# Optimization experiments

Measured on AMD Instinct MI355X. Metric: run time of the kernel, lower is better.

Reference implementation:

```python
import jax, jax.numpy as jnp
import numpy as np
from jax import lax

CUT = 20            # voxel grid per side, hard-coded in the torch module
N, P, OP = 32, 8192, 2048


def _w(key, shape, fan_in):
    return jax.random.normal(key, shape, dtype=jnp.float32) * np.float32(1.0 / np.sqrt(fan_in))


def setup_inputs() -> dict:
    key = jax.random.key(0)
    ks = jax.random.split(key, 20)
    inp = {}
    inp["sc"] = jax.random.uniform(ks[0], (N, P, 2), dtype=jnp.float32, minval=-0.5, maxval=0.5)
    inp["oc"] = jax.random.uniform(ks[1], (N, OP, 2), dtype=jnp.float32, minval=-0.5, maxval=0.5)
    inp["pos"] = jax.random.uniform(ks[2], (N, 2), dtype=jnp.float32, minval=-0.5, maxval=0.5)
    # voxel PointNet MLP (1x1 Conv1d == per-point linear)
    inp["mlp_w1"] = _w(ks[3], (128, 2), 2);        inp["mlp_b1"] = jnp.zeros((128,), jnp.float32)
    inp["mlp_w2"] = _w(ks[4], (256, 128), 128);    inp["mlp_b2"] = jnp.zeros((256,), jnp.float32)
    # dense conv pyramid
    inp["conv1_w"] = _w(ks[5], (512, 256, 3, 3), 256 * 9);   inp["conv1_b"] = jnp.zeros((512,), jnp.float32)
    inp["conv2_w"] = _w(ks[6], (1024, 512, 3, 3), 512 * 9);  inp["conv2_b"] = jnp.zeros((1024,), jnp.float32)
    inp["convt_w"] = _w(ks[7], (512, 1024, 2, 2), 1024 * 4); inp["convt_b"] = jnp.zeros((512,), jnp.float32)
    # object set-abstraction (stack of 1x1 Conv1d)
    inp["sa_w1"] = _w(ks[8], (64, 2), 2);          inp["sa_b1"] = jnp.zeros((64,), jnp.float32)
    inp["sa_w2"] = _w(ks[9], (128, 64), 64);       inp["sa_b2"] = jnp.zeros((128,), jnp.float32)
    inp["sa_w3"] = _w(ks[10], (256, 128), 128);    inp["sa_b3"] = jnp.zeros((256,), jnp.float32)
    inp["sa_w4"] = _w(ks[11], (512, 256), 256);    inp["sa_b4"] = jnp.zeros((512,), jnp.float32)
    # per-cell classifier
    inp["cls_w1"] = _w(ks[12], (1024, 1538), 1538); inp["cls_b1"] = jnp.zeros((1024,), jnp.float32)
    inp["cls_w2"] = _w(ks[13], (256, 1024), 1024);  inp["cls_b2"] = jnp.zeros((256,), jnp.float32)
    inp["cls_w3"] = _w(ks[14], (1, 256), 256);      inp["cls_b3"] = jnp.zeros((1,), jnp.float32)
    return inp


def _conv2d(x, w, b):
    y = lax.conv_general_dilated(x, w, (1, 1), ((1, 1), (1, 1)),
                                 dimension_numbers=("NCHW", "OIHW", "NCHW"))
    return y + b[None, :, None, None]


def _maxpool2(x):
    return lax.reduce_window(x, -jnp.inf, lax.max, (1, 1, 2, 2), (1, 1, 2, 2), "VALID")


def reference(sc, oc, pos,
              mlp_w1, mlp_b1, mlp_w2, mlp_b2,
              conv1_w, conv1_b, conv2_w, conv2_b, convt_w, convt_b,
              sa_w1, sa_b1, sa_w2, sa_b2, sa_w3, sa_b3, sa_w4, sa_b4,
              cls_w1, cls_b1, cls_w2, cls_b2, cls_w3, cls_b3):
    n = sc.shape[0]
    # ---- fused voxelization + PointNet + scatter-max (replaces triple loop) ----
    x, y = sc[..., 0], sc[..., 1]
    # torch condition: cut[i] < x <= cut[i+1] on linspace(-0.5, 0.5, 21)
    bi = jnp.clip(jnp.ceil((x + 0.5) * CUT) - 1, 0, CUT - 1).astype(jnp.int32)
    bj = jnp.clip(jnp.ceil((y + 0.5) * CUT) - 1, 0, CUT - 1).astype(jnp.int32)
    valid = (x > -0.5) & (x <= 0.5) & (y > -0.5) & (y <= 0.5)
    ci = -0.5 + (bi.astype(sc.dtype) + 0.5) / CUT   # voxel center x
    cj = -0.5 + (bj.astype(sc.dtype) + 0.5) / CUT   # voxel center y
    pc = jnp.stack([x - ci, y - cj], axis=-1).reshape(-1, 2)        # [n*P, 2]
    h = jax.nn.relu(pc @ mlp_w1.T + mlp_b1)
    feat = jax.nn.relu(h @ mlp_w2.T + mlp_b2)                       # [n*P, 256]
    seg = jnp.where(valid,
                    jnp.arange(n, dtype=jnp.int32)[:, None] * (CUT * CUT) + bi * CUT + bj,
                    n * CUT * CUT).reshape(-1)                      # invalid -> dummy bin
    nseg = n * CUT * CUT + 1
    mx = jax.ops.segment_max(feat, seg, num_segments=nseg)
    cnt = jax.ops.segment_sum(jnp.ones((n * P,), jnp.float32), seg, num_segments=nseg)
    vox = jnp.where(cnt[:, None] > 0, mx, 0.0)[: n * CUT * CUT]     # empty voxels stay 0
    vox = vox.reshape(n, CUT, CUT, 256).transpose(0, 3, 1, 2)       # [n,256,20,20]
    # ---- dense conv pyramid ----
    f1 = _maxpool2(jax.nn.relu(_conv2d(vox, conv1_w, conv1_b)))     # [n,512,10,10]
    f2 = _maxpool2(jax.nn.relu(_conv2d(f1, conv2_w, conv2_b)))      # [n,1024,5,5]
    f3 = lax.conv_transpose(f2, convt_w, (2, 2), "VALID",
                            dimension_numbers=("NCHW", "OIHW", "NCHW"))
    f3 = f3 + convt_b[None, :, None, None]                          # [n,512,10,10]
    scene = jnp.concatenate([f1, f3], axis=1)                       # [n,1024,10,10]
    S = scene.shape[2]
    scene_flat = scene.reshape(n, 1024, S * S)
    # ---- object PointNet (1x1 convs == per-point linears) + global max ----
    obj_c = oc - jnp.mean(oc, axis=1, keepdims=True)                # [n,OP,2]
    g = jax.nn.relu(obj_c @ sa_w1.T + sa_b1)
    g = jax.nn.relu(g @ sa_w2.T + sa_b2)
    g = jax.nn.relu(g @ sa_w3.T + sa_b3)
    g = jax.nn.relu(g @ sa_w4.T + sa_b4)                            # [n,OP,512]
    obj = jnp.max(g, axis=1)                                        # [n,512]
    obj_tiled = jnp.broadcast_to(obj[:, :, None], (n, 512, S * S))
    # ---- relative position grid ----
    c = -0.5 + (jnp.arange(S, dtype=sc.dtype) + 0.5) / S
    rel_x = jnp.broadcast_to(pos[:, 0][:, None, None] - c[None, :, None], (n, S, S))
    rel_y = jnp.broadcast_to(pos[:, 1][:, None, None] - c[None, None, :], (n, S, S))
    rel = jnp.stack([rel_x, rel_y], axis=1).reshape(n, 2, S * S)
    # ---- per-cell classifier ----
    cin = jnp.concatenate([scene_flat, obj_tiled, rel], axis=1).transpose(0, 2, 1)  # [n,100,1538]
    h = jax.nn.relu(cin @ cls_w1.T + cls_b1)
    h = jax.nn.relu(h @ cls_w2.T + cls_b2)
    return h @ cls_w3.T + cls_b3                                    # [n,100,1]
```

## Files before the change

kernel.cpp:

```cpp
#include <hip/hip_runtime.h>

#define NB 32
#define PP 8192
#define OPP 2048

typedef _Float16 f16;
typedef f16 half8 __attribute__((ext_vector_type(8)));
typedef f16 half4 __attribute__((ext_vector_type(4)));
typedef f16 half2v __attribute__((ext_vector_type(2)));
typedef float f32x4 __attribute__((ext_vector_type(4)));

#define MFMA16(a, b, c) __builtin_amdgcn_mfma_f32_16x16x32_f16(a, b, c, 0, 0, 0)

__global__ __launch_bounds__(256) void prepfuse_k(
    const float* __restrict__ mlp_w2, const float* __restrict__ sa_w2,
    const float* __restrict__ sa_w3, const float* __restrict__ sa_w4,
    const float* __restrict__ cls_w2, const float* __restrict__ cls_w1,
    const float* __restrict__ convt_w, const float* __restrict__ conv1_w,
    const float* __restrict__ conv2_w, const float* __restrict__ oc,
    f16* __restrict__ mw2h, f16* __restrict__ saw2h, f16* __restrict__ saw3h,
    f16* __restrict__ saw4h, f16* __restrict__ cw2h, f16* __restrict__ cw1h,
    f16* __restrict__ ctwh, f16* __restrict__ w1h, f16* __restrict__ w2h,
    float* __restrict__ ocm) {
  __shared__ float tile[512 * 9];
  int bb = blockIdx.x, t = threadIdx.x;
  if (bb < 2048) {
    constexpr int B0 = 8192, B1 = B0 + 2048, B2 = B1 + 8192, B3 = B2 + 32768, B4 = B3 + 65536;
    constexpr int C1e = B4 + 524288;
    constexpr int TOT = C1e + 2097152;
    for (int idx = bb * 256 + t; idx < TOT; idx += 2048 * 256) {
      if (idx < B4) {
        const float* in; f16* out; int off;
        if (idx < B0)      { in = mlp_w2; out = mw2h;  off = idx; }
        else if (idx < B1) { in = sa_w2;  out = saw2h; off = idx - B0; }
        else if (idx < B2) { in = sa_w3;  out = saw3h; off = idx - B1; }
        else if (idx < B3) { in = sa_w4;  out = saw4h; off = idx - B2; }
        else               { in = cls_w2; out = cw2h;  off = idx - B3; }
        float4 v = ((const float4*)in)[off];
        half4 h; h.x = (f16)v.x; h.y = (f16)v.y; h.z = (f16)v.z; h.w = (f16)v.w;
        ((half4*)out)[off] = h;
      } else if (idx < C1e) {
        int i = idx - B4;
        int co = i >> 9, k2 = i & 511;
        float2 v = *(const float2*)(cls_w1 + (size_t)co * 1538 + k2 * 2);
        half2v h = {(f16)v.x, (f16)v.y};
        *(half2v*)(cw1h + (size_t)co * 1024 + k2 * 2) = h;
      } else {
        int i = idx - C1e;
        int j = i & 7, l = (i >> 3) & 63, kb = (i >> 9) & 31, nb = i >> 14;
        int n16 = l & 15, quad = l >> 4;
        int np = nb * 16 + n16;
        int k = kb * 32 + quad * 8 + j;
        int p = np >> 9, o = np & 511;
        ctwh[i] = (f16)convt_w[((size_t)o * 1024 + k) * 4 + (3 - p)];
      }
    }
  } else if (bb < 2080) {
    float* sx = tile; float* sy = tile + 256;
    int n = bb - 2048;
    float ax = 0.f, ay = 0.f;
    for (int p = t; p < OPP; p += 256) {
      ax += oc[((size_t)n * OPP + p) * 2 + 0];
      ay += oc[((size_t)n * OPP + p) * 2 + 1];
    }
    sx[t] = ax; sy[t] = ay;
    __syncthreads();
    for (int s = 128; s > 0; s >>= 1) {
      if (t < s) { sx[t] += sx[t + s]; sy[t] += sy[t + s]; }
      __syncthreads();
    }
    if (t == 0) {
      ocm[n * 2 + 0] = sx[0] / (float)OPP;
      ocm[n * 2 + 1] = sy[0] / (float)OPP;
    }
  } else {
    int co, CI, NBB; const float* src0; f16* wf;
    if (bb < 2592) { co = bb - 2080; CI = 256; NBB = 32; src0 = conv1_w; wf = w1h; }
    else           { co = bb - 2592; CI = 512; NBB = 64; src0 = conv2_w; wf = w2h; }
    const float* src = src0 + (size_t)co * CI * 9;
    for (int i = t; i < CI * 9; i += 256) tile[i] = src[i];
    __syncthreads();
    int nb = co >> 4, l16c = co & 15;
    int tot = (CI / 32) * 9 * 4;
    for (int e = t; e < tot; e += 256) {
      int quad = e & 3;
      int kk = (e >> 2) % 9;
      int cic = e / 36;
      half8 v;
#pragma unroll
      for (int j = 0; j < 8; ++j) v[j] = (f16)tile[(cic * 32 + quad * 8 + j) * 9 + kk];
      *(half8*)(wf + ((((size_t)cic * 9 + kk) * NBB + nb) * 64 + quad * 16 + l16c) * 8) = v;
    }
  }
}

__global__ __launch_bounds__(256) void pointnet_lds_k(
    const float* __restrict__ sc, const float* __restrict__ w1, const float* __restrict__ b1,
    const f16* __restrict__ w2h, const float* __restrict__ b2, float* __restrict__ voxg) {
  __shared__ float voxl[400 * 33];
  int t = threadIdx.x, lane = t & 63, w = t >> 6;
  int quad = lane >> 4, l16 = lane & 15;
  int b = blockIdx.x;
  int ps = b & 3, cg = (b >> 2) & 7, n = b >> 5;
  half2v w1x2[16], w1y2[16], b12[16];
#pragma unroll
  for (int i = 0; i < 16; ++i) {
    int k0 = (i >> 2) * 32 + quad * 8 + (i & 3) * 2;
    w1x2[i] = (half2v){(f16)w1[k0 * 2], (f16)w1[(k0 + 1) * 2]};
    w1y2[i] = (half2v){(f16)w1[k0 * 2 + 1], (f16)w1[(k0 + 1) * 2 + 1]};
    b12[i]  = (half2v){(f16)b1[k0], (f16)b1[k0 + 1]};
  }
  half8 bf[2][4];
  float bias[2];
#pragma unroll
  for (int nt = 0; nt < 2; ++nt) {
    int ch = cg * 32 + nt * 16 + l16;
    bias[nt] = b2[ch];
#pragma unroll
    for (int ks = 0; ks < 4; ++ks)
      bf[nt][ks] = *(const half8*)(w2h + (size_t)ch * 128 + ks * 32 + quad * 8);
  }
  for (int i = t; i < 400 * 33; i += 256) voxl[i] = 0.0f;
  __syncthreads();
  const half2v z2 = {};
  const float* scp = sc + ((size_t)n * PP + (size_t)ps * 2048) * 2;
  int p0 = w * 16 + l16;
  float2 xyA = *(const float2*)(scp + p0 * 2);
  float2 xyB = *(const float2*)(scp + (p0 + 64) * 2);
  for (int it = 0; it < 16; ++it) {
    float xA = xyA.x, yA = xyA.y, xB = xyB.x, yB = xyB.y;
    if (it < 15) {
      xyA = *(const float2*)(scp + ((it + 1) * 128 + p0) * 2);
      xyB = *(const float2*)(scp + ((it + 1) * 128 + p0 + 64) * 2);
    }
    float bifA = fminf(fmaxf(ceilf((xA + 0.5f) * 20.0f) - 1.0f, 0.0f), 19.0f);
    float bjfA = fminf(fmaxf(ceilf((yA + 0.5f) * 20.0f) - 1.0f, 0.0f), 19.0f);
    bool vA = (xA > -0.5f) && (xA <= 0.5f) && (yA > -0.5f) && (yA <= 0.5f);
    float pxA = xA - (-0.5f + (bifA + 0.5f) * 0.05f);
    float pyA = yA - (-0.5f + (bjfA + 0.5f) * 0.05f);
    int bnA = vA ? ((int)bifA * 20 + (int)bjfA) : -1;
    float bifB = fminf(fmaxf(ceilf((xB + 0.5f) * 20.0f) - 1.0f, 0.0f), 19.0f);
    float bjfB = fminf(fmaxf(ceilf((yB + 0.5f) * 20.0f) - 1.0f, 0.0f), 19.0f);
    bool vB = (xB > -0.5f) && (xB <= 0.5f) && (yB > -0.5f) && (yB <= 0.5f);
    float pxB = xB - (-0.5f + (bifB + 0.5f) * 0.05f);
    float pyB = yB - (-0.5f + (bjfB + 0.5f) * 0.05f);
    int bnB = vB ? ((int)bifB * 20 + (int)bjfB) : -1;
    f16 pxhA = (f16)pxA, pyhA = (f16)pyA, pxhB = (f16)pxB, pyhB = (f16)pyB;
    half2v px2A = (half2v){pxhA, pxhA}, py2A = (half2v){pyhA, pyhA};
    half2v px2B = (half2v){pxhB, pxhB}, py2B = (half2v){pyhB, pyhB};
    f32x4 acc0A = {}, acc1A = {}, acc0B = {}, acc1B = {};
#pragma unroll
    for (int ks = 0; ks < 4; ++ks) {
      half8 afA, afB;
#pragma unroll
      for (int j2 = 0; j2 < 4; ++j2) {
        half2v wx = w1x2[ks * 4 + j2], wy = w1y2[ks * 4 + j2], bb = b12[ks * 4 + j2];
        half2v tA = wx * px2A + (wy * py2A + bb);
        half2v tB = wx * px2B + (wy * py2B + bb);
        reinterpret_cast<half2v*>(&afA)[j2] = __builtin_elementwise_max(tA, z2);
        reinterpret_cast<half2v*>(&afB)[j2] = __builtin_elementwise_max(tB, z2);
      }
      acc0A = MFMA16(afA, bf[0][ks], acc0A);
      acc0B = MFMA16(afB, bf[0][ks], acc0B);
      acc1A = MFMA16(afA, bf[1][ks], acc1A);
      acc1B = MFMA16(afB, bf[1][ks], acc1B);
    }
#pragma unroll
    for (int r = 0; r < 4; ++r) {
      int bnA2 = __shfl(bnA, quad * 4 + r);
      int bnB2 = __shfl(bnB, quad * 4 + r);
      if (bnA2 >= 0) {
        float v0 = fmaxf(acc0A[r] + bias[0], 0.0f);
        float v1 = fmaxf(acc1A[r] + bias[1], 0.0f);
        atomicMax((int*)voxl + bnA2 * 33 + l16, __float_as_int(v0));
        atomicMax((int*)voxl + bnA2 * 33 + 16 + l16, __float_as_int(v1));
      }
      if (bnB2 >= 0) {
        float v0 = fmaxf(acc0B[r] + bias[0], 0.0f);
        float v1 = fmaxf(acc1B[r] + bias[1], 0.0f);
        atomicMax((int*)voxl + bnB2 * 33 + l16, __float_as_int(v0));
        atomicMax((int*)voxl + bnB2 * 33 + 16 + l16, __float_as_int(v1));
      }
    }
  }
  __syncthreads();
  float* vg = voxg + ((size_t)n * 400) * 256 + cg * 32;
  for (int i = t; i < 400 * 32; i += 256) {
    int bin = i >> 5, c = i & 31;
    float v = voxl[bin * 33 + c];
    if (v > 0.0f)
      atomicMax((int*)(vg + (size_t)bin * 256) + c, __float_as_int(v));
  }
}

template <int H, int W, int CI, int CO, int MSPLIT, int NIMG, bool INF32, bool WR2>
__global__ __launch_bounds__(256) void convpool_k(
    const void* __restrict__ inv, const f16* __restrict__ wf,
    const float* __restrict__ bias, f16* __restrict__ out1, f16* __restrict__ out2) {
  constexpr int HS = H / MSPLIT;
  constexpr int IMGPIX = HS * W;
  constexpr int Mpix = NIMG * IMGPIX;
  constexpr int MT = (Mpix + 15) / 16;
  constexpr int PR = HS + 2, PC = W + 2;
  constexpr int CELLS = NIMG * PR * PC;
  constexpr int NCIC = CI / 32;
  constexpr int COG = CO / 128;
  constexpr int NBB = CO / 16;
  constexpr int PW = W / 2;
  constexpr int POPS = (H / 2) * (W / 2);
  extern __shared__ char smem[];
  f16* Ap = (f16*)smem;
  f16* pb = (f16*)smem;
  int b = blockIdx.x;
  int cog = b % COG;
  int ms = (b / COG) % MSPLIT;
  int n0 = (b / (COG * MSPLIT)) * NIMG;
  int co0 = cog * 128;
  int r0 = ms * HS;
  int t = threadIdx.x, lane = t & 63, w = t >> 6;
  int quad = lane >> 4, l16 = lane & 15;
  int nb0 = cog * 8 + w * 2;

  int abase[MT];
#pragma unroll
  for (int mi = 0; mi < MT; ++mi) {
    int pl = mi * 16 + l16; if (pl > Mpix - 1) pl = Mpix - 1;
    int img = pl / IMGPIX, lp = pl - img * IMGPIX;
    int y = lp / W, x = lp - y * W;
    abase[mi] = ((img * PR * PC) + y * PC + x) * 40 + quad * 8;
  }
  f32x4 acc[MT][2] = {};

  for (int cic = 0; cic < NCIC; ++cic) {
    __syncthreads();
    for (int cell = t; cell < CELLS; cell += 256) {
      int img = cell / (PR * PC), rc = cell - img * (PR * PC);
      int pr = rc / PC, pc = rc - pr * PC;
      int yin = r0 - 1 + pr, xin = pc - 1;
      if constexpr (INF32) {
        half8 v[4] = {};
        if (yin >= 0 && yin < H && xin >= 0 && xin < W) {
          const float4* src = (const float4*)((const float*)inv +
              (size_t)(n0 + img) * H * W * CI + ((size_t)yin * W + xin) * CI + cic * 32);
#pragma unroll
          for (int j = 0; j < 4; ++j) {
            float4 a = src[j * 2], c = src[j * 2 + 1];
            v[j][0] = (f16)a.x; v[j][1] = (f16)a.y; v[j][2] = (f16)a.z; v[j][3] = (f16)a.w;
            v[j][4] = (f16)c.x; v[j][5] = (f16)c.y; v[j][6] = (f16)c.z; v[j][7] = (f16)c.w;
          }
        }
        half8* dst = (half8*)(Ap + cell * 40);
        dst[0] = v[0]; dst[1] = v[1]; dst[2] = v[2]; dst[3] = v[3];
      } else {
        uint4 d0 = {0,0,0,0}, d1 = {0,0,0,0}, d2 = {0,0,0,0}, d3 = {0,0,0,0};
        if (yin >= 0 && yin < H && xin >= 0 && xin < W) {
          const uint4* src = (const uint4*)((const f16*)inv +
              (size_t)(n0 + img) * H * W * CI + ((size_t)yin * W + xin) * CI + cic * 32);
          d0 = src[0]; d1 = src[1]; d2 = src[2]; d3 = src[3];
        }
        uint4* dst = (uint4*)(Ap + cell * 40);
        dst[0] = d0; dst[1] = d1; dst[2] = d2; dst[3] = d3;
      }
    }
    __syncthreads();
    const f16* wfc = wf + (size_t)(cic * 9) * NBB * 512;
#pragma unroll
    for (int ky = 0; ky < 3; ++ky)
#pragma unroll
      for (int kx = 0; kx < 3; ++kx) {
        int kk = ky * 3 + kx;
        half8 bf0 = *(const half8*)(wfc + ((size_t)(kk * NBB + nb0) * 64 + lane) * 8);
        half8 bf1 = *(const half8*)(wfc + ((size_t)(kk * NBB + nb0 + 1) * 64 + lane) * 8);
        int shift = (ky * PC + kx) * 40;
#pragma unroll
        for (int mi = 0; mi < MT; ++mi) {
          half8 af = *(const half8*)(Ap + abase[mi] + shift);
          acc[mi][0] = MFMA16(af, bf0, acc[mi][0]);
          acc[mi][1] = MFMA16(af, bf1, acc[mi][1]);
        }
      }
  }
  int co_w = co0 + w * 32;
  float bv0 = bias[co_w + l16];
  float bv1 = bias[co_w + 16 + l16];
  __syncthreads();
#pragma unroll
  for (int mi = 0; mi < MT; ++mi)
#pragma unroll
    for (int r = 0; r < 4; ++r) {
      int p = mi * 16 + quad * 4 + r;
      if (p < Mpix) {
        float v0 = acc[mi][0][r] + bv0; v0 = v0 > 0.f ? v0 : 0.f;
        float v1 = acc[mi][1][r] + bv1; v1 = v1 > 0.f ? v1 : 0.f;
        pb[p * 136 + w * 32 + l16] = (f16)v0;
        pb[p * 136 + w * 32 + 16 + l16] = (f16)v1;
      }
    }
  __syncthreads();
  for (int i = t; i < NIMG * PW * 64; i += 256) {
    int c2 = (i & 63) * 2;
    int rem = i >> 6;
    int px = rem % PW, img = rem / PW;
    int b00 = (img * IMGPIX + 2 * px) * 136 + c2;
    int b10 = (img * IMGPIX + W + 2 * px) * 136 + c2;
    float a0 = fmaxf((float)pb[b00], (float)pb[b00 + 136]);
    float a1 = fmaxf((float)pb[b00 + 1], (float)pb[b00 + 137]);
    float c0 = fmaxf((float)pb[b10], (float)pb[b10 + 136]);
    float c1 = fmaxf((float)pb[b10 + 1], (float)pb[b10 + 137]);
    union { f16 h[2]; unsigned u; } pk;
    pk.h[0] = (f16)fmaxf(a0, c0);
    pk.h[1] = (f16)fmaxf(a1, c1);
    size_t op = (size_t)(n0 + img) * POPS + ms * PW + px;
    *(unsigned*)(out1 + op * CO + co0 + c2) = pk.u;
    if constexpr (WR2)
      *(unsigned*)(out2 + op * 1024 + co0 + c2) = pk.u;
  }
}

__global__ __launch_bounds__(256, 2) void convt_mfma_k(
    const f16* __restrict__ f2h, const f16* __restrict__ ctwf,
    const float* __restrict__ ctb, f16* __restrict__ scnh) {
  __shared__ f16 act[25 * 1048];
  int b = blockIdx.x;
  int ng = b & 15, n = b >> 4;
  int t = threadIdx.x, lane = t & 63, w = t >> 6;
  int quad = lane >> 4, l16 = lane & 15;
  for (int i = t; i < 25 * 128; i += 256) {
    int row = i >> 7, c8 = i & 127;
    *(half8*)(act + row * 1048 + c8 * 8) =
        *(const half8*)(f2h + ((size_t)n * 25 + row) * 1024 + c8 * 8);
  }
  __syncthreads();
  int r1 = 16 + (l16 > 8 ? 8 : l16);
  f32x4 acc[2][2] = {};
  const f16* wp0 = ctwf + ((size_t)((ng * 8 + w * 2 + 0) * 32) * 64 + lane) * 8;
  const f16* wp1 = ctwf + ((size_t)((ng * 8 + w * 2 + 1) * 32) * 64 + lane) * 8;
#pragma unroll 4
  for (int ks = 0; ks < 32; ++ks) {
    half8 a0 = *(const half8*)(act + l16 * 1048 + ks * 32 + quad * 8);
    half8 a1 = *(const half8*)(act + r1 * 1048 + ks * 32 + quad * 8);
    half8 b0 = *(const half8*)(wp0 + (size_t)ks * 512);
    half8 b1 = *(const half8*)(wp1 + (size_t)ks * 512);
    acc[0][0] = MFMA16(a0, b0, acc[0][0]);
    acc[1][0] = MFMA16(a1, b0, acc[1][0]);
    acc[0][1] = MFMA16(a0, b1, acc[0][1]);
    acc[1][1] = MFMA16(a1, b1, acc[1][1]);
  }
#pragma unroll
  for (int nt = 0; nt < 2; ++nt) {
    int np = ng * 128 + w * 32 + nt * 16 + l16;
    int p = np >> 9, co = np & 511;
    int a = p >> 1, bc = p & 1;
    float bb = ctb[co];
#pragma unroll
    for (int mt = 0; mt < 2; ++mt)
#pragma unroll
      for (int r = 0; r < 4; ++r) {
        int px = mt * 16 + quad * 4 + r;
        if (px < 25) {
          int ph = px / 5, pw = px - ph * 5;
          int opx = (2 * ph + a) * 10 + 2 * pw + bc;
          scnh[((size_t)n * 100 + opx) * 1024 + 512 + co] = (f16)(acc[mt][nt][r] + bb);
        }
      }
  }
}

__global__ __launch_bounds__(256, 2) void sa_mfma_k(
    const float* __restrict__ oc, const float* __restrict__ ocm,
    const float* __restrict__ w1, const float* __restrict__ b1,
    const f16* __restrict__ w2h, const float* __restrict__ b2,
    const f16* __restrict__ w3h, const float* __restrict__ b3,
    const f16* __restrict__ w4h, const float* __restrict__ b4,
    float* __restrict__ obj) {
  __shared__ f16 act1[64 * 72];
  __shared__ f16 act2[64 * 136];
  __shared__ f16 act3[64 * 264];
  __shared__ float pcx[64], pcy[64];
  int b = blockIdx.x;
  int n = b >> 5, pb = (b & 31) * 64;
  int t = threadIdx.x, lane = t & 63, w = t >> 6;
  int quad = lane >> 4, l16 = lane & 15;
  if (t < 64) {
    pcx[t] = oc[((size_t)n * OPP + pb + t) * 2 + 0] - ocm[n * 2 + 0];
    pcy[t] = oc[((size_t)n * OPP + pb + t) * 2 + 1] - ocm[n * 2 + 1];
  }
  __syncthreads();
  {
    int c = t & 63, pg = t >> 6;
    float wx = w1[c * 2], wy = w1[c * 2 + 1], bb = b1[c];
#pragma unroll
    for (int j = 0; j < 16; ++j) {
      int p = pg * 16 + j;
      act1[p * 72 + c] = (f16)fmaxf(fmaf(wx, pcx[p], fmaf(wy, pcy[p], bb)), 0.0f);
    }
  }
  __syncthreads();
  {
    int n0 = w * 32;
    f32x4 acc[4][2] = {};
#pragma unroll
    for (int ks = 0; ks < 2; ++ks) {
      half8 a[4];
#pragma unroll
      for (int mt = 0; mt < 4; ++mt)
        a[mt] = *(const half8*)(act1 + (mt * 16 + l16) * 72 + ks * 32 + quad * 8);
#pragma unroll
      for (int nt = 0; nt < 2; ++nt) {
        half8 bf = *(const half8*)(w2h + (size_t)(n0 + nt * 16 + l16) * 64 + ks * 32 + quad * 8);
#pragma unroll
        for (int mt = 0; mt < 4; ++mt)
          acc[mt][nt] = MFMA16(a[mt], bf, acc[mt][nt]);
      }
    }
#pragma unroll
    for (int nt = 0; nt < 2; ++nt) {
      int col = n0 + nt * 16 + l16;
      float bb = b2[col];
#pragma unroll
      for (int mt = 0; mt < 4; ++mt)
#pragma unroll
        for (int r = 0; r < 4; ++r)
          act2[(mt * 16 + quad * 4 + r) * 136 + col] = (f16)fmaxf(acc[mt][nt][r] + bb, 0.0f);
    }
  }
  __syncthreads();
  {
    int n0 = w * 64;
    f32x4 acc[4][4] = {};
#pragma unroll
    for (int ks = 0; ks < 4; ++ks) {
      half8 a[4];
#pragma unroll
      for (int mt = 0; mt < 4; ++mt)
        a[mt] = *(const half8*)(act2 + (mt * 16 + l16) * 136 + ks * 32 + quad * 8);
#pragma unroll
      for (int nt = 0; nt < 4; ++nt) {
        half8 bf = *(const half8*)(w3h + (size_t)(n0 + nt * 16 + l16) * 128 + ks * 32 + quad * 8);
#pragma unroll
        for (int mt = 0; mt < 4; ++mt)
          acc[mt][nt] = MFMA16(a[mt], bf, acc[mt][nt]);
      }
    }
#pragma unroll
    for (int nt = 0; nt < 4; ++nt) {
      int col = n0 + nt * 16 + l16;
      float bb = b3[col];
#pragma unroll
      for (int mt = 0; mt < 4; ++mt)
#pragma unroll
        for (int r = 0; r < 4; ++r)
          act3[(mt * 16 + quad * 4 + r) * 264 + col] = (f16)fmaxf(acc[mt][nt][r] + bb, 0.0f);
    }
  }
  __syncthreads();
  {
    int n0 = w * 128;
    f32x4 acc[4][8] = {};
#pragma unroll
    for (int ks = 0; ks < 8; ++ks) {
      half8 a[4];
#pragma unroll
      for (int mt = 0; mt < 4; ++mt)
        a[mt] = *(const half8*)(act3 + (mt * 16 + l16) * 264 + ks * 32 + quad * 8);
#pragma unroll
      for (int nt = 0; nt < 8; ++nt) {
        half8 bf = *(const half8*)(w4h + (size_t)(n0 + nt * 16 + l16) * 256 + ks * 32 + quad * 8);
#pragma unroll
        for (int mt = 0; mt < 4; ++mt)
          acc[mt][nt] = MFMA16(a[mt], bf, acc[mt][nt]);
      }
    }
#pragma unroll
    for (int nt = 0; nt < 8; ++nt) {
      int col = n0 + nt * 16 + l16;
      float bb = b4[col];
      float v = 0.0f;
#pragma unroll
      for (int mt = 0; mt < 4; ++mt)
#pragma unroll
        for (int r = 0; r < 4; ++r)
          v = fmaxf(v, acc[mt][nt][r] + bb);
      v = fmaxf(v, 0.0f);
      v = fmaxf(v, __shfl_xor(v, 16));
      v = fmaxf(v, __shfl_xor(v, 32));
      if (quad == 0)
        atomicMax((int*)obj + (size_t)n * 512 + col, __float_as_int(v));
    }
  }
}

__global__ __launch_bounds__(256) void odprep_k(
    const float* __restrict__ obj, const float* __restrict__ w1raw,
    const float* __restrict__ b1, float* __restrict__ odw, float* __restrict__ wab) {
  int co = blockIdx.x;
  int t = threadIdx.x, lane = t & 63, w = t >> 6;
  const float* wr = w1raw + (size_t)co * 1538 + 1024;
  float2 wv[4];
#pragma unroll
  for (int j = 0; j < 4; ++j) wv[j] = *(const float2*)(wr + lane * 8 + j * 2);
  float bb = b1[co];
  for (int i = 0; i < 8; ++i) {
    int n = w * 8 + i;
    const float* ob = obj + (size_t)n * 512 + lane * 8;
    float od = 0.0f;
#pragma unroll
    for (int j = 0; j < 4; ++j) {
      float2 ov = *(const float2*)(ob + j * 2);
      od = fmaf(wv[j].x, ov.x, od);
      od = fmaf(wv[j].y, ov.y, od);
    }
    od += __shfl_xor(od, 1);  od += __shfl_xor(od, 2);
    od += __shfl_xor(od, 4);  od += __shfl_xor(od, 8);
    od += __shfl_xor(od, 16); od += __shfl_xor(od, 32);
    if (lane == 0) odw[(size_t)n * 1024 + co] = od + bb;
  }
  if (t == 0) { wab[co * 2] = wr[512]; wab[co * 2 + 1] = wr[513]; }
}

__global__ __launch_bounds__(256) void cls1_mfma_k(
    const f16* __restrict__ scnh, const float* __restrict__ odw,
    const float* __restrict__ wab, const float* __restrict__ pos,
    const f16* __restrict__ w1h, f16* __restrict__ h1h) {
  __shared__ f16 act[25 * 1032];
  __shared__ float odl[128], wAl[128], wBl[128];
  int b = blockIdx.x;
  int o8 = b & 7, mq = (b >> 3) & 3, n = b >> 5;
  int co0 = o8 * 128, p0 = mq * 25;
  int t = threadIdx.x, lane = t & 63, w = t >> 6;
  int quad = lane >> 4, l16 = lane & 15;
  for (int i = t; i < 25 * 128; i += 256) {
    int row = i >> 7, c8 = i & 127;
    *(half8*)(act + row * 1032 + c8 * 8) =
        *(const half8*)(scnh + ((size_t)n * 100 + p0 + row) * 1024 + c8 * 8);
  }
  if (t < 128) {
    odl[t] = odw[(size_t)n * 1024 + co0 + t];
    float2 ab = *(const float2*)(wab + (size_t)(co0 + t) * 2);
    wAl[t] = ab.x; wBl[t] = ab.y;
  }
  __syncthreads();
  float posx = pos[n * 2 + 0], posy = pos[n * 2 + 1];
  f32x4 acc[2][2];
#pragma unroll
  for (int mt = 0; mt < 2; ++mt)
#pragma unroll
    for (int nt = 0; nt < 2; ++nt) {
      int cl = w * 32 + nt * 16 + l16;
      float od = odl[cl], wA = wAl[cl], wB = wBl[cl];
#pragma unroll
      for (int r = 0; r < 4; ++r) {
        int pl = mt * 16 + quad * 4 + r;
        int px = p0 + (pl < 25 ? pl : 24);
        float relx = posx - (-0.5f + ((px / 10) + 0.5f) * 0.1f);
        float rely = posy - (-0.5f + ((px % 10) + 0.5f) * 0.1f);
        acc[mt][nt][r] = od + relx * wA + rely * wB;
      }
    }
  int gr0 = l16;
  int gr1 = (16 + l16 > 24) ? 24 : 16 + l16;
  const f16* wb0 = w1h + (size_t)(co0 + w * 32 + l16) * 1024 + quad * 8;
  const f16* wb1 = wb0 + (size_t)16 * 1024;
#pragma unroll 4
  for (int kq = 0; kq < 32; ++kq) {
    int k0 = kq * 32;
    half8 bf0 = *(const half8*)(wb0 + k0);
    half8 bf1 = *(const half8*)(wb1 + k0);
    half8 a0 = *(const half8*)(act + gr0 * 1032 + k0 + quad * 8);
    half8 a1 = *(const half8*)(act + gr1 * 1032 + k0 + quad * 8);
    acc[0][0] = MFMA16(a0, bf0, acc[0][0]);
    acc[1][0] = MFMA16(a1, bf0, acc[1][0]);
    acc[0][1] = MFMA16(a0, bf1, acc[0][1]);
    acc[1][1] = MFMA16(a1, bf1, acc[1][1]);
  }
#pragma unroll
  for (int mt = 0; mt < 2; ++mt)
#pragma unroll
    for (int nt = 0; nt < 2; ++nt) {
      int co = co0 + w * 32 + nt * 16 + l16;
#pragma unroll
      for (int r = 0; r < 4; ++r) {
        int pl = mt * 16 + quad * 4 + r;
        if (pl < 25)
          h1h[((size_t)n * 100 + p0 + pl) * 1024 + co] = (f16)fmaxf(acc[mt][nt][r], 0.0f);
      }
    }
}

__global__ __launch_bounds__(256) void cls2_mfma_k(
    const f16* __restrict__ h1h, const f16* __restrict__ w2h16,
    const float* __restrict__ b2, f16* __restrict__ h2h) {
  __shared__ f16 act[25 * 1032];
  int b = blockIdx.x;
  int ng = b & 1, mq = (b >> 1) & 3, n = b >> 3;
  int co0 = ng * 128, p0 = mq * 25;
  int t = threadIdx.x, lane = t & 63, w = t >> 6;
  int quad = lane >> 4, l16 = lane & 15;
  for (int i = t; i < 25 * 128; i += 256) {
    int row = i >> 7, c8 = i & 127;
    *(half8*)(act + row * 1032 + c8 * 8) =
        *(const half8*)(h1h + ((size_t)n * 100 + p0 + row) * 1024 + c8 * 8);
  }
  __syncthreads();
  f32x4 acc[2][2] = {};
  int gr0 = l16;
  int gr1 = (16 + l16 > 24) ? 24 : 16 + l16;
  const f16* wb0 = w2h16 + (size_t)(co0 + w * 32 + l16) * 1024 + quad * 8;
  const f16* wb1 = wb0 + (size_t)16 * 1024;
#pragma unroll 4
  for (int kq = 0; kq < 32; ++kq) {
    int k0 = kq * 32;
    half8 bf0 = *(const half8*)(wb0 + k0);
    half8 bf1 = *(const half8*)(wb1 + k0);
    half8 a0 = *(const half8*)(act + gr0 * 1032 + k0 + quad * 8);
    half8 a1 = *(const half8*)(act + gr1 * 1032 + k0 + quad * 8);
    acc[0][0] = MFMA16(a0, bf0, acc[0][0]);
    acc[1][0] = MFMA16(a1, bf0, acc[1][0]);
    acc[0][1] = MFMA16(a0, bf1, acc[0][1]);
    acc[1][1] = MFMA16(a1, bf1, acc[1][1]);
  }
#pragma unroll
  for (int mt = 0; mt < 2; ++mt)
#pragma unroll
    for (int nt = 0; nt < 2; ++nt) {
      int co = co0 + w * 32 + nt * 16 + l16;
      float bb = b2[co];
#pragma unroll
      for (int r = 0; r < 4; ++r) {
        int pl = mt * 16 + quad * 4 + r;
        if (pl < 25)
          h2h[((size_t)n * 100 + p0 + pl) * 256 + co] = (f16)fmaxf(acc[mt][nt][r] + bb, 0.0f);
      }
    }
}

__global__ void cls3_k(const f16* __restrict__ h2h, const float* __restrict__ w3,
                       const float* __restrict__ b3, float* __restrict__ out) {
  int n = blockIdx.x, t = threadIdx.x;
  if (t < 100) {
    float acc = b3[0];
    const f16* hp = &h2h[((size_t)n * 100 + t) * 256];
    for (int k = 0; k < 256; ++k) acc = fmaf((float)hp[k], w3[k], acc);
    out[n * 100 + t] = acc;
  }
}

extern "C" void kernel_launch(void* const* d_in, const int* in_sizes, int n_in,
                              void* d_out, int out_size, void* d_ws, size_t ws_size,
                              hipStream_t stream) {
  const float* sc      = (const float*)d_in[0];
  const float* oc      = (const float*)d_in[1];
  const float* pos     = (const float*)d_in[2];
  const float* mlp_w1  = (const float*)d_in[3];
  const float* mlp_b1  = (const float*)d_in[4];
  const float* mlp_w2  = (const float*)d_in[5];
  const float* mlp_b2  = (const float*)d_in[6];
  const float* conv1_w = (const float*)d_in[7];
  const float* conv1_b = (const float*)d_in[8];
  const float* conv2_w = (const float*)d_in[9];
  const float* conv2_b = (const float*)d_in[10];
  const float* convt_w = (const float*)d_in[11];
  const float* convt_b = (const float*)d_in[12];
  const float* sa_w1   = (const float*)d_in[13];
  const float* sa_b1   = (const float*)d_in[14];
  const float* sa_w2   = (const float*)d_in[15];
  const float* sa_b2   = (const float*)d_in[16];
  const float* sa_w3   = (const float*)d_in[17];
  const float* sa_b3   = (const float*)d_in[18];
  const float* sa_w4   = (const float*)d_in[19];
  const float* sa_b4   = (const float*)d_in[20];
  const float* cls_w1  = (const float*)d_in[21];
  const float* cls_b1  = (const float*)d_in[22];
  const float* cls_w2  = (const float*)d_in[23];
  const float* cls_b2  = (const float*)d_in[24];
  const float* cls_w3  = (const float*)d_in[25];
  const float* cls_b3  = (const float*)d_in[26];

  float* ws = (float*)d_ws;
  f16*   w1h   = (f16*)ws;
  f16*   w2h   = (f16*)(ws + 589824);
  f16*   mw2h  = (f16*)(ws + 2949120);
  f16*   saw2h = (f16*)(ws + 2965504);
  f16*   saw3h = (f16*)(ws + 2969600);
  f16*   saw4h = (f16*)(ws + 2985984);
  f16*   cw1h  = (f16*)(ws + 3051520);
  f16*   ctwh  = (f16*)(ws + 3575808);
  f16*   cw2h  = (f16*)(ws + 4624384);
  float* obj   = ws + 4870144;
  float* big   = ws + 4886528;
  f16*   voxh  = (f16*)(ws + 8163328);
  f16*   f1h   = (f16*)(ws + 8982528);
  f16*   scnh  = (f16*)(ws + 9801728);
  float* ocm   = ws + 11456512;

  float* voxg  = big;
  f16*   f2h   = voxh;
  f16*   h1h   = w2h;
  f16*   h2h   = scnh;
  float* odw   = big + 2097152;
  float* wab   = big + 2129920;
  float* outp  = (float*)d_out;

  hipMemsetAsync(obj, 0, (size_t)(16384 + 3276800) * 4, stream);
  prepfuse_k<<<3616, 256, 0, stream>>>(mlp_w2, sa_w2, sa_w3, sa_w4, cls_w2, cls_w1,
                                       convt_w, conv1_w, conv2_w, oc,
                                       mw2h, saw2h, saw3h, saw4h, cw2h, cw1h,
                                       ctwh, w1h, w2h, ocm);

  pointnet_lds_k<<<1024, 256, 0, stream>>>(sc, mlp_w1, mlp_b1, mw2h, mlp_b2, voxg);

  convpool_k<20, 20, 256, 512, 10, 2, true, true><<<640, 256, 21760, stream>>>(
      voxg, w1h, conv1_b, f1h, scnh);
  convpool_k<10, 10, 512, 1024, 5, 2, false, false><<<640, 256, 10880, stream>>>(
      f1h, w2h, conv2_b, f2h, nullptr);

  convt_mfma_k<<<512, 256, 0, stream>>>(f2h, ctwh, convt_b, scnh);

  sa_mfma_k<<<1024, 256, 0, stream>>>(oc, ocm, sa_w1, sa_b1, saw2h, sa_b2,
                                      saw3h, sa_b3, saw4h, sa_b4, obj);
  odprep_k<<<1024, 256, 0, stream>>>(obj, cls_w1, cls_b1, odw, wab);

  cls1_mfma_k<<<1024, 256, 0, stream>>>(scnh, odw, wab, pos, cw1h, h1h);
  cls2_mfma_k<<<256, 256, 0, stream>>>(h1h, cw2h, cls_b2, h2h);
  cls3_k<<<32, 128, 0, stream>>>(h2h, cls_w3, cls_b3, outp);
}
```

Baseline: 445.1 us.

## Merge independent stages into horizontally fused kernels to cut launches

Folds weight preprocessing, the object-mean reduction and the scene PointNet into one kernel, dispatching on block index, so pointnet converts mlp_w2 to half inline. Conv1 and the object set-abstraction MLP now share a launch, as do the transposed conv and the object-dot prep. This removes several kernel launches and lets independent work overlap on the GPU. The cost is a larger shared-memory footprint per block (the fused kernels size LDS for the biggest role) and more register pressure, which may lower occupancy for the smaller roles.

```diff
diff --git a/kernel.cpp b/kernel.cpp
--- a/kernel.cpp
+++ b/kernel.cpp
@@ -12,95 +12,12 @@
 
 #define MFMA16(a, b, c) __builtin_amdgcn_mfma_f32_16x16x32_f16(a, b, c, 0, 0, 0)
 
-__global__ __launch_bounds__(256) void prepfuse_k(
-    const float* __restrict__ mlp_w2, const float* __restrict__ sa_w2,
-    const float* __restrict__ sa_w3, const float* __restrict__ sa_w4,
-    const float* __restrict__ cls_w2, const float* __restrict__ cls_w1,
-    const float* __restrict__ convt_w, const float* __restrict__ conv1_w,
-    const float* __restrict__ conv2_w, const float* __restrict__ oc,
-    f16* __restrict__ mw2h, f16* __restrict__ saw2h, f16* __restrict__ saw3h,
-    f16* __restrict__ saw4h, f16* __restrict__ cw2h, f16* __restrict__ cw1h,
-    f16* __restrict__ ctwh, f16* __restrict__ w1h, f16* __restrict__ w2h,
-    float* __restrict__ ocm) {
-  __shared__ float tile[512 * 9];
-  int bb = blockIdx.x, t = threadIdx.x;
-  if (bb < 2048) {
-    constexpr int B0 = 8192, B1 = B0 + 2048, B2 = B1 + 8192, B3 = B2 + 32768, B4 = B3 + 65536;
-    constexpr int C1e = B4 + 524288;
-    constexpr int TOT = C1e + 2097152;
-    for (int idx = bb * 256 + t; idx < TOT; idx += 2048 * 256) {
-      if (idx < B4) {
-        const float* in; f16* out; int off;
-        if (idx < B0)      { in = mlp_w2; out = mw2h;  off = idx; }
-        else if (idx < B1) { in = sa_w2;  out = saw2h; off = idx - B0; }
-        else if (idx < B2) { in = sa_w3;  out = saw3h; off = idx - B1; }
-        else if (idx < B3) { in = sa_w4;  out = saw4h; off = idx - B2; }
-        else               { in = cls_w2; out = cw2h;  off = idx - B3; }
-        float4 v = ((const float4*)in)[off];
-        half4 h; h.x = (f16)v.x; h.y = (f16)v.y; h.z = (f16)v.z; h.w = (f16)v.w;
-        ((half4*)out)[off] = h;
-      } else if (idx < C1e) {
-        int i = idx - B4;
-        int co = i >> 9, k2 = i & 511;
-        float2 v = *(const float2*)(cls_w1 + (size_t)co * 1538 + k2 * 2);
-        half2v h = {(f16)v.x, (f16)v.y};
-        *(half2v*)(cw1h + (size_t)co * 1024 + k2 * 2) = h;
-      } else {
-        int i = idx - C1e;
-        int j = i & 7, l = (i >> 3) & 63, kb = (i >> 9) & 31, nb = i >> 14;
-        int n16 = l & 15, quad = l >> 4;
-        int np = nb * 16 + n16;
-        int k = kb * 32 + quad * 8 + j;
-        int p = np >> 9, o = np & 511;
-        ctwh[i] = (f16)convt_w[((size_t)o * 1024 + k) * 4 + (3 - p)];
-      }
-    }
-  } else if (bb < 2080) {
-    float* sx = tile; float* sy = tile + 256;
-    int n = bb - 2048;
-    float ax = 0.f, ay = 0.f;
-    for (int p = t; p < OPP; p += 256) {
-      ax += oc[((size_t)n * OPP + p) * 2 + 0];
-      ay += oc[((size_t)n * OPP + p) * 2 + 1];
-    }
-    sx[t] = ax; sy[t] = ay;
-    __syncthreads();
-    for (int s = 128; s > 0; s >>= 1) {
-      if (t < s) { sx[t] += sx[t + s]; sy[t] += sy[t + s]; }
-      __syncthreads();
-    }
-    if (t == 0) {
-      ocm[n * 2 + 0] = sx[0] / (float)OPP;
-      ocm[n * 2 + 1] = sy[0] / (float)OPP;
-    }
-  } else {
-    int co, CI, NBB; const float* src0; f16* wf;
-    if (bb < 2592) { co = bb - 2080; CI = 256; NBB = 32; src0 = conv1_w; wf = w1h; }
-    else           { co = bb - 2592; CI = 512; NBB = 64; src0 = conv2_w; wf = w2h; }
-    const float* src = src0 + (size_t)co * CI * 9;
-    for (int i = t; i < CI * 9; i += 256) tile[i] = src[i];
-    __syncthreads();
-    int nb = co >> 4, l16c = co & 15;
-    int tot = (CI / 32) * 9 * 4;
-    for (int e = t; e < tot; e += 256) {
-      int quad = e & 3;
-      int kk = (e >> 2) % 9;
-      int cic = e / 36;
-      half8 v;
-#pragma unroll
-      for (int j = 0; j < 8; ++j) v[j] = (f16)tile[(cic * 32 + quad * 8 + j) * 9 + kk];
-      *(half8*)(wf + ((((size_t)cic * 9 + kk) * NBB + nb) * 64 + quad * 16 + l16c) * 8) = v;
-    }
-  }
-}
-
-__global__ __launch_bounds__(256) void pointnet_lds_k(
-    const float* __restrict__ sc, const float* __restrict__ w1, const float* __restrict__ b1,
-    const f16* __restrict__ w2h, const float* __restrict__ b2, float* __restrict__ voxg) {
-  __shared__ float voxl[400 * 33];
+__device__ __forceinline__ void pointnet_body(
+    int b, float* voxl, const float* __restrict__ sc, const float* __restrict__ w1,
+    const float* __restrict__ b1, const float* __restrict__ w2raw,
+    const float* __restrict__ b2, float* __restrict__ voxg) {
   int t = threadIdx.x, lane = t & 63, w = t >> 6;
   int quad = lane >> 4, l16 = lane & 15;
-  int b = blockIdx.x;
   int ps = b & 3, cg = (b >> 2) & 7, n = b >> 5;
   half2v w1x2[16], w1y2[16], b12[16];
 #pragma unroll
@@ -117,8 +34,13 @@
     int ch = cg * 32 + nt * 16 + l16;
     bias[nt] = b2[ch];
 #pragma unroll
-    for (int ks = 0; ks < 4; ++ks)
-      bf[nt][ks] = *(const half8*)(w2h + (size_t)ch * 128 + ks * 32 + quad * 8);
+    for (int ks = 0; ks < 4; ++ks) {
+      half8 v;
+#pragma unroll
+      for (int j = 0; j < 8; ++j)
+        v[j] = (f16)w2raw[(size_t)ch * 128 + ks * 32 + quad * 8 + j];
+      bf[nt][ks] = v;
+    }
   }
   for (int i = t; i < 400 * 33; i += 256) voxl[i] = 0.0f;
   __syncthreads();
@@ -193,9 +115,96 @@
   }
 }
 
+__global__ __launch_bounds__(256) void fuse1_k(
+    const float* __restrict__ sc, const float* __restrict__ mlp_w1,
+    const float* __restrict__ mlp_b1, const float* __restrict__ mlp_w2,
+    const float* __restrict__ mlp_b2,
+    const float* __restrict__ sa_w2, const float* __restrict__ sa_w3,
+    const float* __restrict__ sa_w4, const float* __restrict__ cls_w2,
+    const float* __restrict__ cls_w1, const float* __restrict__ convt_w,
+    const float* __restrict__ conv1_w, const float* __restrict__ conv2_w,
+    const float* __restrict__ oc,
+    f16* __restrict__ saw2h, f16* __restrict__ saw3h, f16* __restrict__ saw4h,
+    f16* __restrict__ cw2h, f16* __restrict__ cw1h, f16* __restrict__ ctwh,
+    f16* __restrict__ w1h, f16* __restrict__ w2h,
+    float* __restrict__ ocm, float* __restrict__ voxg) {
+  __shared__ float shf[13200];
+  int bb = blockIdx.x, t = threadIdx.x;
+  if (bb < 1024) {
+    pointnet_body(bb, shf, sc, mlp_w1, mlp_b1, mlp_w2, mlp_b2, voxg);
+  } else if (bb < 3072) {
+    constexpr int B0 = 2048, B1 = B0 + 8192, B2 = B1 + 32768, B3 = B2 + 65536;
+    constexpr int C1e = B3 + 524288;
+    constexpr int TOT = C1e + 2097152;
+    for (int idx = (bb - 1024) * 256 + t; idx < TOT; idx += 2048 * 256) {
+      if (idx < B3) {
+        const float* in; f16* out; int off;
+        if (idx < B0)      { in = sa_w2;  out = saw2h; off = idx; }
+        else if (idx < B1) { in = sa_w3;  out = saw3h; off = idx - B0; }
+        else if (idx < B2) { in = sa_w4;  out = saw4h; off = idx - B1; }
+        else               { in = cls_w2; out = cw2h;  off = idx - B2; }
+        float4 v = ((const float4*)in)[off];
+        half4 h; h.x = (f16)v.x; h.y = (f16)v.y; h.z = (f16)v.z; h.w = (f16)v.w;
+        ((half4*)out)[off] = h;
+      } else if (idx < C1e) {
+        int i = idx - B3;
+        int co = i >> 9, k2 = i & 511;
+        float2 v = *(const float2*)(cls_w1 + (size_t)co * 1538 + k2 * 2);
+        half2v h = {(f16)v.x, (f16)v.y};
+        *(half2v*)(cw1h + (size_t)co * 1024 + k2 * 2) = h;
+      } else {
+        int i = idx - C1e;
+        int j = i & 7, l = (i >> 3) & 63, kb = (i >> 9) & 31, nb = i >> 14;
+        int n16 = l & 15, quad = l >> 4;
+        int np = nb * 16 + n16;
+        int k = kb * 32 + quad * 8 + j;
+        int p = np >> 9, o = np & 511;
+        ctwh[i] = (f16)convt_w[((size_t)o * 1024 + k) * 4 + (3 - p)];
+      }
+    }
+  } else if (bb < 3104) {
+    float* sx = shf; float* sy = shf + 256;
+    int n = bb - 3072;
+    float ax = 0.f, ay = 0.f;
+    for (int p = t; p < OPP; p += 256) {
+      ax += oc[((size_t)n * OPP + p) * 2 + 0];
+      ay += oc[((size_t)n * OPP + p) * 2 + 1];
+    }
+    sx[t] = ax; sy[t] = ay;
+    __syncthreads();
+    for (int s = 128; s > 0; s >>= 1) {
+      if (t < s) { sx[t] += sx[t + s]; sy[t] += sy[t + s]; }
+      __syncthreads();
+    }
+    if (t == 0) {
+      ocm[n * 2 + 0] = sx[0] / (float)OPP;
+      ocm[n * 2 + 1] = sy[0] / (float)OPP;
+    }
+  } else {
+    float* tile = shf;
+    int co, CI, NBB; const float* src0; f16* wf;
+    if (bb < 3616) { co = bb - 3104; CI = 256; NBB = 32; src0 = conv1_w; wf = w1h; }
+    else           { co = bb - 3616; CI = 512; NBB = 64; src0 = conv2_w; wf = w2h; }
+    const float* src = src0 + (size_t)co * CI * 9;
+    for (int i = t; i < CI * 9; i += 256) tile[i] = src[i];
+    __syncthreads();
+    int nb = co >> 4, l16c = co & 15;
+    int tot = (CI / 32) * 9 * 4;
+    for (int e = t; e < tot; e += 256) {
+      int quad = e & 3;
+      int kk = (e >> 2) % 9;
+      int cic = e / 36;
+      half8 v;
+#pragma unroll
+      for (int j = 0; j < 8; ++j) v[j] = (f16)tile[(cic * 32 + quad * 8 + j) * 9 + kk];
+      *(half8*)(wf + ((((size_t)cic * 9 + kk) * NBB + nb) * 64 + quad * 16 + l16c) * 8) = v;
+    }
+  }
+}
+
 template <int H, int W, int CI, int CO, int MSPLIT, int NIMG, bool INF32, bool WR2>
-__global__ __launch_bounds__(256) void convpool_k(
-    const void* __restrict__ inv, const f16* __restrict__ wf,
+__device__ __forceinline__ void convpool_body(
+    int b, char* smem, const void* __restrict__ inv, const f16* __restrict__ wf,
     const float* __restrict__ bias, f16* __restrict__ out1, f16* __restrict__ out2) {
   constexpr int HS = H / MSPLIT;
   constexpr int IMGPIX = HS * W;
@@ -208,10 +217,8 @@
   constexpr int NBB = CO / 16;
   constexpr int PW = W / 2;
   constexpr int POPS = (H / 2) * (W / 2);
-  extern __shared__ char smem[];
   f16* Ap = (f16*)smem;
   f16* pb = (f16*)smem;
-  int b = blockIdx.x;
   int cog = b % COG;
   int ms = (b / COG) % MSPLIT;
   int n0 = (b / (COG * MSPLIT)) * NIMG;
@@ -317,67 +324,26 @@
   }
 }
 
-__global__ __launch_bounds__(256, 2) void convt_mfma_k(
-    const f16* __restrict__ f2h, const f16* __restrict__ ctwf,
-    const float* __restrict__ ctb, f16* __restrict__ scnh) {
-  __shared__ f16 act[25 * 1048];
-  int b = blockIdx.x;
-  int ng = b & 15, n = b >> 4;
-  int t = threadIdx.x, lane = t & 63, w = t >> 6;
-  int quad = lane >> 4, l16 = lane & 15;
-  for (int i = t; i < 25 * 128; i += 256) {
-    int row = i >> 7, c8 = i & 127;
-    *(half8*)(act + row * 1048 + c8 * 8) =
-        *(const half8*)(f2h + ((size_t)n * 25 + row) * 1024 + c8 * 8);
-  }
-  __syncthreads();
-  int r1 = 16 + (l16 > 8 ? 8 : l16);
-  f32x4 acc[2][2] = {};
-  const f16* wp0 = ctwf + ((size_t)((ng * 8 + w * 2 + 0) * 32) * 64 + lane) * 8;
-  const f16* wp1 = ctwf + ((size_t)((ng * 8 + w * 2 + 1) * 32) * 64 + lane) * 8;
-#pragma unroll 4
-  for (int ks = 0; ks < 32; ++ks) {
-    half8 a0 = *(const half8*)(act + l16 * 1048 + ks * 32 + quad * 8);
-    half8 a1 = *(const half8*)(act + r1 * 1048 + ks * 32 + quad * 8);
-    half8 b0 = *(const half8*)(wp0 + (size_t)ks * 512);
-    half8 b1 = *(const half8*)(wp1 + (size_t)ks * 512);
-    acc[0][0] = MFMA16(a0, b0, acc[0][0]);
-    acc[1][0] = MFMA16(a1, b0, acc[1][0]);
-    acc[0][1] = MFMA16(a0, b1, acc[0][1]);
-    acc[1][1] = MFMA16(a1, b1, acc[1][1]);
-  }
-#pragma unroll
-  for (int nt = 0; nt < 2; ++nt) {
-    int np = ng * 128 + w * 32 + nt * 16 + l16;
-    int p = np >> 9, co = np & 511;
-    int a = p >> 1, bc = p & 1;
-    float bb = ctb[co];
-#pragma unroll
-    for (int mt = 0; mt < 2; ++mt)
-#pragma unroll
-      for (int r = 0; r < 4; ++r) {
-        int px = mt * 16 + quad * 4 + r;
-        if (px < 25) {
-          int ph = px / 5, pw = px - ph * 5;
-          int opx = (2 * ph + a) * 10 + 2 * pw + bc;
-          scnh[((size_t)n * 100 + opx) * 1024 + 512 + co] = (f16)(acc[mt][nt][r] + bb);
-        }
-      }
-  }
-}
-
-__global__ __launch_bounds__(256, 2) void sa_mfma_k(
-    const float* __restrict__ oc, const float* __restrict__ ocm,
+template <int H, int W, int CI, int CO, int MSPLIT, int NIMG, bool INF32, bool WR2>
+__global__ __launch_bounds__(256) void convpool_k(
+    const void* __restrict__ inv, const f16* __restrict__ wf,
+    const float* __restrict__ bias, f16* __restrict__ out1, f16* __restrict__ out2) {
+  extern __shared__ char smem[];
+  convpool_body<H, W, CI, CO, MSPLIT, NIMG, INF32, WR2>(blockIdx.x, smem, inv, wf, bias, out1, out2);
+}
+
+__device__ __forceinline__ void sa_body(
+    int b, char* smem, const float* __restrict__ oc, const float* __restrict__ ocm,
     const float* __restrict__ w1, const float* __restrict__ b1,
     const f16* __restrict__ w2h, const float* __restrict__ b2,
     const f16* __restrict__ w3h, const float* __restrict__ b3,
     const f16* __restrict__ w4h, const float* __restrict__ b4,
     float* __restrict__ obj) {
-  __shared__ f16 act1[64 * 72];
-  __shared__ f16 act2[64 * 136];
-  __shared__ f16 act3[64 * 264];
-  __shared__ float pcx[64], pcy[64];
-  int b = blockIdx.x;
+  f16* act1 = (f16*)smem;
+  f16* act2 = (f16*)(smem + 9216);
+  f16* act3 = (f16*)(smem + 26624);
+  float* pcx = (float*)(smem + 60416);
+  float* pcy = (float*)(smem + 60672);
   int n = b >> 5, pb = (b & 31) * 64;
   int t = threadIdx.x, lane = t & 63, w = t >> 6;
   int quad = lane >> 4, l16 = lane & 15;
@@ -490,32 +456,98 @@
   }
 }
 
-__global__ __launch_bounds__(256) void odprep_k(
+__global__ __launch_bounds__(256, 2) void fuse2_k(
+    const float* __restrict__ voxg, const f16* __restrict__ w1h,
+    const float* __restrict__ conv1_b, f16* __restrict__ f1h, f16* __restrict__ scnh,
+    const float* __restrict__ oc, const float* __restrict__ ocm,
+    const float* __restrict__ sa_w1, const float* __restrict__ sa_b1,
+    const f16* __restrict__ saw2h, const float* __restrict__ sa_b2,
+    const f16* __restrict__ saw3h, const float* __restrict__ sa_b3,
+    const f16* __restrict__ saw4h, const float* __restrict__ sa_b4,
+    float* __restrict__ obj) {
+  extern __shared__ char smem[];
+  if (blockIdx.x < 640)
+    convpool_body<20, 20, 256, 512, 10, 2, true, true>(blockIdx.x, smem, voxg, w1h,
+                                                       conv1_b, f1h, scnh);
+  else
+    sa_body(blockIdx.x - 640, smem, oc, ocm, sa_w1, sa_b1, saw2h, sa_b2,
+            saw3h, sa_b3, saw4h, sa_b4, obj);
+}
+
+__global__ __launch_bounds__(256) void fuse3_k(
+    const f16* __restrict__ f2h, const f16* __restrict__ ctwf,
+    const float* __restrict__ ctb, f16* __restrict__ scnh,
     const float* __restrict__ obj, const float* __restrict__ w1raw,
     const float* __restrict__ b1, float* __restrict__ odw, float* __restrict__ wab) {
-  int co = blockIdx.x;
+  __shared__ f16 act[25 * 1048];
+  int bb = blockIdx.x;
   int t = threadIdx.x, lane = t & 63, w = t >> 6;
-  const float* wr = w1raw + (size_t)co * 1538 + 1024;
-  float2 wv[4];
-#pragma unroll
-  for (int j = 0; j < 4; ++j) wv[j] = *(const float2*)(wr + lane * 8 + j * 2);
-  float bb = b1[co];
-  for (int i = 0; i < 8; ++i) {
-    int n = w * 8 + i;
-    const float* ob = obj + (size_t)n * 512 + lane * 8;
-    float od = 0.0f;
-#pragma unroll
-    for (int j = 0; j < 4; ++j) {
-      float2 ov = *(const float2*)(ob + j * 2);
-      od = fmaf(wv[j].x, ov.x, od);
-      od = fmaf(wv[j].y, ov.y, od);
-    }
-    od += __shfl_xor(od, 1);  od += __shfl_xor(od, 2);
-    od += __shfl_xor(od, 4);  od += __shfl_xor(od, 8);
-    od += __shfl_xor(od, 16); od += __shfl_xor(od, 32);
-    if (lane == 0) odw[(size_t)n * 1024 + co] = od + bb;
-  }
-  if (t == 0) { wab[co * 2] = wr[512]; wab[co * 2 + 1] = wr[513]; }
+  int quad = lane >> 4, l16 = lane & 15;
+  if (bb < 512) {
+    int ng = bb & 15, n = bb >> 4;
+    for (int i = t; i < 25 * 128; i += 256) {
+      int row = i >> 7, c8 = i & 127;
+      *(half8*)(act + row * 1048 + c8 * 8) =
+          *(const half8*)(f2h + ((size_t)n * 25 + row) * 1024 + c8 * 8);
+    }
+    __syncthreads();
+    int r1 = 16 + (l16 > 8 ? 8 : l16);
+    f32x4 acc[2][2] = {};
+    const f16* wp0 = ctwf + ((size_t)((ng * 8 + w * 2 + 0) * 32) * 64 + lane) * 8;
+    const f16* wp1 = ctwf + ((size_t)((ng * 8 + w * 2 + 1) * 32) * 64 + lane) * 8;
+#pragma unroll 4
+    for (int ks = 0; ks < 32; ++ks) {
+      half8 a0 = *(const half8*)(act + l16 * 1048 + ks * 32 + quad * 8);
+      half8 a1 = *(const half8*)(act + r1 * 1048 + ks * 32 + quad * 8);
+      half8 b0 = *(const half8*)(wp0 + (size_t)ks * 512);
+      half8 b1 = *(const half8*)(wp1 + (size_t)ks * 512);
+      acc[0][0] = MFMA16(a0, b0, acc[0][0]);
+      acc[1][0] = MFMA16(a1, b0, acc[1][0]);
+      acc[0][1] = MFMA16(a0, b1, acc[0][1]);
+      acc[1][1] = MFMA16(a1, b1, acc[1][1]);
+    }
+#pragma unroll
+    for (int nt = 0; nt < 2; ++nt) {
+      int np = ng * 128 + w * 32 + nt * 16 + l16;
+      int p = np >> 9, co = np & 511;
+      int a = p >> 1, bc = p & 1;
+      float bb2 = ctb[co];
+#pragma unroll
+      for (int mt = 0; mt < 2; ++mt)
+#pragma unroll
+        for (int r = 0; r < 4; ++r) {
+          int px = mt * 16 + quad * 4 + r;
+          if (px < 25) {
+            int ph = px / 5, pw = px - ph * 5;
+            int opx = (2 * ph + a) * 10 + 2 * pw + bc;
+            scnh[((size_t)n * 100 + opx) * 1024 + 512 + co] = (f16)(acc[mt][nt][r] + bb2);
+          }
+        }
+    }
+  } else {
+    int co = bb - 512;
+    const float* wr = w1raw + (size_t)co * 1538 + 1024;
+    float2 wv[4];
+#pragma unroll
+    for (int j = 0; j < 4; ++j) wv[j] = *(const float2*)(wr + lane * 8 + j * 2);
+    float bb2 = b1[co];
+    for (int i = 0; i < 8; ++i) {
+      int n = w * 8 + i;
+      const float* ob = obj + (size_t)n * 512 + lane * 8;
+      float od = 0.0f;
+#pragma unroll
+      for (int j = 0; j < 4; ++j) {
+        float2 ov = *(const float2*)(ob + j * 2);
+        od = fmaf(wv[j].x, ov.x, od);
+        od = fmaf(wv[j].y, ov.y, od);
+      }
+      od += __shfl_xor(od, 1);  od += __shfl_xor(od, 2);
+      od += __shfl_xor(od, 4);  od += __shfl_xor(od, 8);
+      od += __shfl_xor(od, 16); od += __shfl_xor(od, 32);
+      if (lane == 0) odw[(size_t)n * 1024 + co] = od + bb2;
+    }
+    if (t == 0) { wab[co * 2] = wr[512]; wab[co * 2 + 1] = wr[513]; }
+  }
 }
 
 __global__ __launch_bounds__(256) void cls1_mfma_k(
@@ -679,7 +711,6 @@
   float* ws = (float*)d_ws;
   f16*   w1h   = (f16*)ws;
   f16*   w2h   = (f16*)(ws + 589824);
-  f16*   mw2h  = (f16*)(ws + 2949120);
   f16*   saw2h = (f16*)(ws + 2965504);
   f16*   saw3h = (f16*)(ws + 2969600);
   f16*   saw4h = (f16*)(ws + 2985984);
@@ -702,23 +733,22 @@
   float* outp  = (float*)d_out;
 
   hipMemsetAsync(obj, 0, (size_t)(16384 + 3276800) * 4, stream);
-  prepfuse_k<<<3616, 256, 0, stream>>>(mlp_w2, sa_w2, sa_w3, sa_w4, cls_w2, cls_w1,
-                                       convt_w, conv1_w, conv2_w, oc,
-                                       mw2h, saw2h, saw3h, saw4h, cw2h, cw1h,
-                                       ctwh, w1h, w2h, ocm);
-
-  pointnet_lds_k<<<1024, 256, 0, stream>>>(sc, mlp_w1, mlp_b1, mw2h, mlp_b2, voxg);
-
-  convpool_k<20, 20, 256, 512, 10, 2, true, true><<<640, 256, 21760, stream>>>(
-      voxg, w1h, conv1_b, f1h, scnh);
+
+  fuse1_k<<<4640, 256, 0, stream>>>(sc, mlp_w1, mlp_b1, mlp_w2, mlp_b2,
+                                    sa_w2, sa_w3, sa_w4, cls_w2, cls_w1, convt_w,
+                                    conv1_w, conv2_w, oc,
+                                    saw2h, saw3h, saw4h, cw2h, cw1h, ctwh,
+                                    w1h, w2h, ocm, voxg);
+
+  fuse2_k<<<1664, 256, 60928, stream>>>(voxg, w1h, conv1_b, f1h, scnh,
+                                        oc, ocm, sa_w1, sa_b1, saw2h, sa_b2,
+                                        saw3h, sa_b3, saw4h, sa_b4, obj);
+
   convpool_k<10, 10, 512, 1024, 5, 2, false, false><<<640, 256, 10880, stream>>>(
       f1h, w2h, conv2_b, f2h, nullptr);
 
-  convt_mfma_k<<<512, 256, 0, stream>>>(f2h, ctwh, convt_b, scnh);
-
-  sa_mfma_k<<<1024, 256, 0, stream>>>(oc, ocm, sa_w1, sa_b1, saw2h, sa_b2,
-                                      saw3h, sa_b3, saw4h, sa_b4, obj);
-  odprep_k<<<1024, 256, 0, stream>>>(obj, cls_w1, cls_b1, odw, wab);
+  fuse3_k<<<1536, 256, 0, stream>>>(f2h, ctwh, convt_b, scnh, obj, cls_w1, cls_b1,
+                                    odw, wab);
 
   cls1_mfma_k<<<1024, 256, 0, stream>>>(scnh, odw, wab, pos, cw1h, h1h);
   cls2_mfma_k<<<256, 256, 0, stream>>>(h1h, cw2h, cls_b2, h2h);
```

New measurement: 451.2 us. No clear change (+1.4%).
